# Kernel tuning notes

Hardware: AMD Instinct MI355X
Metric: run time of the kernel (lower is better)

Reference implementation:

```python
import jax, jax.numpy as jnp
import numpy as np

B, E, C, K, H, OUT = 8192, 16, 256, 2, 64, 387

def setup_inputs() -> dict:
    ks = jax.random.split(jax.random.key(0), 6)
    x = jax.random.normal(ks[0], (B, E, C), dtype=jnp.float32)
    adj = jax.random.normal(ks[1], (E, E), dtype=jnp.float32) * (6.0 / (E + E)) ** 0.5  # xavier-ish
    adj_bias = jax.random.normal(ks[2], (1,), dtype=jnp.float32) * 0.1
    cheb_w = jax.random.normal(ks[3], (K * C, H), dtype=jnp.float32) * (6.0 / (K * C + H)) ** 0.5
    brelu_bias = jnp.zeros((1, 1, H), dtype=jnp.float32)
    fc_w = jax.random.normal(ks[4], (OUT, H), dtype=jnp.float32) * (1.0 / H) ** 0.5
    fc_b = jax.random.normal(ks[5], (OUT,), dtype=jnp.float32) * (1.0 / H) ** 0.5
    return {"x": x, "adj": adj, "adj_bias": adj_bias, "cheb_w": cheb_w,
            "brelu_bias": brelu_bias, "fc_w": fc_w, "fc_b": fc_b}

def reference(x, adj, adj_bias, cheb_w, brelu_bias, fc_w, fc_b):
    # adaptive adjacency + biased ReLU (Eq. 4 prelude)
    w = jax.nn.relu(adj + adj_bias)  # (E,E)
    # normalized Laplacian: I - D^{-1/2} W D^{-1/2}
    d_re = 1.0 / jnp.sqrt(jnp.sum(w, axis=1) + 1e-5)  # (E,)
    lap = jnp.eye(E, dtype=x.dtype) - d_re[:, None] * w * d_re[None, :]  # (E,E)
    # Chebyshev polynomial, k=2: T0 = ones, T1 = lap @ x
    t0 = jnp.ones_like(x)                       # (B,E,C)
    t1 = jnp.einsum('ij,bjc->bic', lap, x)      # (B,E,C)
    # torch: stack on dim=1 -> permute(0,2,3,1) -> flatten(2)  == interleave along last axis
    cp = jnp.stack([t0, t1], axis=-1).reshape(B, E, K * C)  # (B,E,K*C)
    h = jnp.einsum('bek,kh->beh', cp, cheb_w)   # (B,E,H)
    # dropout is identity at eval
    h = jax.nn.relu(brelu_bias + h)
    out = jnp.einsum('beh,oh->beo', h, fc_w) + fc_b  # (B,E,OUT)
    return out
```

## Files before the change

kernel.cpp:

```cpp
#include <hip/hip_runtime.h>
#include <stdint.h>


typedef __attribute__((ext_vector_type(4))) float f32x4;
typedef __attribute__((ext_vector_type(8))) short s16x8;
typedef __attribute__((ext_vector_type(4))) short s16x4;

#define WS_CH_B    0
#define WS_LAP_B   256
#define WS_LAPA_B  1280
#define WS_FCB_B   1792
#define WS_W1T2_B  4096
#define WS_FCW2_B  36864

static __device__ __forceinline__ short f2bf(float f) {
    union { float f; uint32_t u; } v; v.f = f;
    uint32_t r = (v.u + 0x7fffu + ((v.u >> 16) & 1u)) >> 16;
    return (short)r;
}

__global__ void prep_kernel(const float* __restrict__ adj,
                            const float* __restrict__ adj_bias,
                            const float* __restrict__ cheb_w,
                            const float* __restrict__ brelu_bias,
                            const float* __restrict__ fc_w,
                            const float* __restrict__ fc_b,
                            char* __restrict__ ws) {
    float* chf  = (float*)(ws + WS_CH_B);
    float* lapf = (float*)(ws + WS_LAP_B);
    short* lapA = (short*)(ws + WS_LAPA_B);
    float* fcbp = (float*)(ws + WS_FCB_B);
    short* w1t2 = (short*)(ws + WS_W1T2_B);
    short* fcw2 = (short*)(ws + WS_FCW2_B);
    int t = threadIdx.x;

    if (blockIdx.x == 0) {
        __shared__ float sw[16][17];
        __shared__ float sdre[16];
        __shared__ float slap[16][16];
        __shared__ float csum[4][64];
        float ab = adj_bias[0];
        {
            int i = t >> 4, j = t & 15;
            sw[i][j] = fmaxf(adj[t] + ab, 0.f);
        }
        {
            int hh = t & 63, part = t >> 6;
            float s = 0.f;
            #pragma unroll 8
            for (int i = 0; i < 64; ++i) s += cheb_w[(2 * (part * 64 + i)) * 64 + hh];
            csum[part][hh] = s;
        }
        __syncthreads();
        if (t < 16) {
            float s = 0.f;
            #pragma unroll
            for (int j = 0; j < 16; ++j) s += sw[t][j];
            sdre[t] = 1.0f / sqrtf(s + 1e-5f);
        }
        __syncthreads();
        {
            int i = t >> 4, j = t & 15;
            float l = (i == j ? 1.f : 0.f) - sdre[i] * sw[i][j] * sdre[j];
            slap[i][j] = l;
            lapf[t] = l;
        }
        __syncthreads();
        if (t < 64) {
            int m = t & 15, qq = t >> 4;
            #pragma unroll
            for (int i = 0; i < 4; ++i)
                lapA[t * 4 + i] = f2bf(slap[m][qq * 4 + i]);
            chf[t] = csum[0][t] + csum[1][t] + csum[2][t] + csum[3][t] + brelu_bias[t];
        }
        for (int o = t; o < 400; o += 256) fcbp[o] = (o < 387) ? fc_b[o] : 0.f;
    }
    int gt = blockIdx.x * blockDim.x + t;
    int nthr = gridDim.x * blockDim.x;
    for (int idx = gt; idx < 32 * 512; idx += nthr) {
        int frag = idx >> 9, r = idx & 511;
        int lane = r >> 3, j = r & 7;
        int kb = frag >> 2, nt = frag & 3;
        int k = kb * 32 + (lane >> 4) * 8 + j;
        int col = nt * 16 + (lane & 15);
        w1t2[idx] = f2bf(cheb_w[(2 * k + 1) * 64 + col]);
    }
    for (int idx = gt; idx < 50 * 512; idx += nthr) {
        int frag = idx >> 9, r = idx & 511;
        int lane = r >> 3, j = r & 7;
        int tt = frag >> 1, f = frag & 1;
        int o = tt * 16 + (lane & 15);
        int k = f * 32 + (lane >> 4) * 8 + j;
        fcw2[idx] = (o < 387) ? f2bf(fc_w[o * 64 + k]) : (short)0;
    }
}

__global__ __launch_bounds__(256) void fused_kernel(
        const float* __restrict__ x,
        const char* __restrict__ ws,
        float* __restrict__ out) {
    const float* chf  = (const float*)(ws + WS_CH_B);
    const short* lapA = (const short*)(ws + WS_LAPA_B);
    const float* fcbp = (const float*)(ws + WS_FCB_B);
    const short* w1t2 = (const short*)(ws + WS_W1T2_B);
    const short* fcw2 = (const short*)(ws + WS_FCW2_B);

    __shared__ __align__(16) short sw1[32 * 512];
    __shared__ __align__(16) short hs[4][16][80];

    const int lane = threadIdx.x & 63;
    const int wave = threadIdx.x >> 6;
    const int n = lane & 15;
    const int q = lane >> 4;
    const long b = (long)blockIdx.x * 4 + wave;

    {
        const s16x8* srcv = (const s16x8*)w1t2;
        s16x8* dstv = (s16x8*)sw1;
        #pragma unroll
        for (int i = 0; i < 8; ++i)
            dstv[i * 256 + threadIdx.x] = srcv[i * 256 + threadIdx.x];
    }

    const float* xrow = x + b * 4096 + n * 256 + q * 8;
    f32x4 xr[16];
    #pragma unroll
    for (int kb = 0; kb < 8; ++kb) {
        xr[2 * kb]     = *(const f32x4*)(xrow + kb * 32);
        xr[2 * kb + 1] = *(const f32x4*)(xrow + kb * 32 + 4);
    }
    s16x8 af[8];
    #pragma unroll
    for (int kb = 0; kb < 8; ++kb) {
        f32x4 xa = xr[2 * kb], xc = xr[2 * kb + 1];
        af[kb][0] = f2bf(xa[0]); af[kb][1] = f2bf(xa[1]);
        af[kb][2] = f2bf(xa[2]); af[kb][3] = f2bf(xa[3]);
        af[kb][4] = f2bf(xc[0]); af[kb][5] = f2bf(xc[1]);
        af[kb][6] = f2bf(xc[2]); af[kb][7] = f2bf(xc[3]);
    }
    __syncthreads();

    const short* w1l = sw1 + lane * 8;
    s16x8 bfr[2][4];
    #pragma unroll
    for (int nt = 0; nt < 4; ++nt)
        bfr[0][nt] = *(const s16x8*)(w1l + nt * 512);
    f32x4 g[4];
    #pragma unroll
    for (int nt = 0; nt < 4; ++nt) g[nt] = (f32x4){0.f, 0.f, 0.f, 0.f};
    #pragma unroll
    for (int kb = 0; kb < 8; ++kb) {
        const int cur = kb & 1;
        if (kb < 7) {
            #pragma unroll
            for (int nt = 0; nt < 4; ++nt)
                bfr[cur ^ 1][nt] = *(const s16x8*)(w1l + ((kb + 1) * 4 + nt) * 512);
        }
        #pragma unroll
        for (int nt = 0; nt < 4; ++nt)
            g[nt] = __builtin_amdgcn_mfma_f32_16x16x32_bf16(af[kb], bfr[cur][nt], g[nt], 0, 0, 0);
    }

    f32x4 h[4];
#if defined(__has_builtin) && __has_builtin(__builtin_amdgcn_mfma_f32_16x16x16bf16_1k)
    {
        s16x4 la = *(const s16x4*)(lapA + lane * 4);
        const f32x4 z4 = (f32x4){0.f, 0.f, 0.f, 0.f};
        #pragma unroll
        for (int nt = 0; nt < 4; ++nt) {
            s16x4 gb;
            gb[0] = f2bf(g[nt][0]); gb[1] = f2bf(g[nt][1]);
            gb[2] = f2bf(g[nt][2]); gb[3] = f2bf(g[nt][3]);
            h[nt] = __builtin_amdgcn_mfma_f32_16x16x16bf16_1k(la, gb, z4, 0, 0, 0);
        }
    }
#else
    {
        __shared__ float gs[4][16][68];
        const float* lapf = (const float*)(ws + WS_LAP_B);
        #pragma unroll
        for (int r = 0; r < 4; ++r) {
            gs[wave][q * 4 + r][0 * 16 + n] = g[0][r];
            gs[wave][q * 4 + r][1 * 16 + n] = g[1][r];
            gs[wave][q * 4 + r][2 * 16 + n] = g[2][r];
            gs[wave][q * 4 + r][3 * 16 + n] = g[3][r];
        }
        __syncthreads();
        #pragma unroll
        for (int nt = 0; nt < 4; ++nt) h[nt] = (f32x4){0.f, 0.f, 0.f, 0.f};
        #pragma unroll
        for (int e = 0; e < 16; ++e) {
            float l0 = lapf[(q * 4 + 0) * 16 + e];
            float l1 = lapf[(q * 4 + 1) * 16 + e];
            float l2 = lapf[(q * 4 + 2) * 16 + e];
            float l3 = lapf[(q * 4 + 3) * 16 + e];
            #pragma unroll
            for (int nt = 0; nt < 4; ++nt) {
                float gv = gs[wave][e][nt * 16 + n];
                h[nt][0] += l0 * gv; h[nt][1] += l1 * gv;
                h[nt][2] += l2 * gv; h[nt][3] += l3 * gv;
            }
        }
    }
#endif

    #pragma unroll
    for (int nt = 0; nt < 4; ++nt) {
        float cv = chf[nt * 16 + n];
        #pragma unroll
        for (int r = 0; r < 4; ++r) {
            float v = fmaxf(h[nt][r] + cv, 0.f);
            hs[wave][q * 4 + r][nt * 16 + n] = f2bf(v);
        }
    }

    const short* fw = fcw2 + lane * 8;
    s16x8 fb[2][2];
    {
        const int tt0 = wave;
        fb[0][0] = *(const s16x8*)(fw + (tt0 * 2 + 0) * 512);
        fb[0][1] = *(const s16x8*)(fw + (tt0 * 2 + 1) * 512);
    }
    asm volatile("s_waitcnt lgkmcnt(0)" ::: "memory");
    __builtin_amdgcn_s_barrier();
    __builtin_amdgcn_sched_barrier(0);

    s16x8 ha[4][2];
    #pragma unroll
    for (int gi = 0; gi < 4; ++gi) {
        ha[gi][0] = *(const s16x8*)(&hs[gi][n][q * 8]);
        ha[gi][1] = *(const s16x8*)(&hs[gi][n][32 + q * 8]);
    }

    const long bbase = (long)blockIdx.x * 4;
    #pragma unroll
    for (int i = 0; i < 7; ++i) {
        const int tt = wave + 4 * i;
        if (tt >= 25) break;
        const int cur = i & 1;
        const int tn = tt + 4;
        if (tn < 25) {
            fb[cur ^ 1][0] = *(const s16x8*)(fw + (tn * 2 + 0) * 512);
            fb[cur ^ 1][1] = *(const s16x8*)(fw + (tn * 2 + 1) * 512);
        }
        const int o = tt * 16 + n;
        const float bias = fcbp[o];
        #pragma unroll
        for (int gi = 0; gi < 4; ++gi) {
            f32x4 acc = (f32x4){bias, bias, bias, bias};
            acc = __builtin_amdgcn_mfma_f32_16x16x32_bf16(ha[gi][0], fb[cur][0], acc, 0, 0, 0);
            acc = __builtin_amdgcn_mfma_f32_16x16x32_bf16(ha[gi][1], fb[cur][1], acc, 0, 0, 0);
            if (o < 387) {
                float* outb = out + ((bbase + gi) * 16 + q * 4) * 387;
                outb[0 * 387 + o] = acc[0];
                outb[1 * 387 + o] = acc[1];
                outb[2 * 387 + o] = acc[2];
                outb[3 * 387 + o] = acc[3];
            }
        }
    }
}

extern "C" void kernel_launch(void* const* d_in, const int* in_sizes, int n_in,
                              void* d_out, int out_size, void* d_ws, size_t ws_size,
                              hipStream_t stream) {
    const float* x          = (const float*)d_in[0];
    const float* adj        = (const float*)d_in[1];
    const float* adj_bias   = (const float*)d_in[2];
    const float* cheb_w     = (const float*)d_in[3];
    const float* brelu_bias = (const float*)d_in[4];
    const float* fc_w       = (const float*)d_in[5];
    const float* fc_b       = (const float*)d_in[6];
    float* outp = (float*)d_out;
    char* ws = (char*)d_ws;

    prep_kernel<<<64, 256, 0, stream>>>(adj, adj_bias, cheb_w, brelu_bias, fc_w, fc_b, ws);
    fused_kernel<<<2048, 256, 0, stream>>>(x, ws, outp);
}
```

Baseline: 343.0 us.

## Process two batch groups per block and prefetch next x tile during compute

Each block now handles two groups of four batch elements instead of one and launches half as many blocks. The shared cheb weight staging, Laplacian fragment, bias and channel constants are loaded once and reused for both groups. The second group's x rows are loaded from global memory while the first group's MFMA work is running. This spreads the per-block setup cost over more work and hides load latency, but it raises register pressure and adds a barrier between the two iterations.

```diff
diff --git a/kernel.cpp b/kernel.cpp
--- a/kernel.cpp
+++ b/kernel.cpp
@@ -112,7 +112,17 @@
     const int wave = threadIdx.x >> 6;
     const int n = lane & 15;
     const int q = lane >> 4;
-    const long b = (long)blockIdx.x * 4 + wave;
+
+    const long grp0 = (long)blockIdx.x * 2;
+    f32x4 xr[16];
+    {
+        const float* xrow = x + (grp0 * 4 + wave) * 4096 + n * 256 + q * 8;
+        #pragma unroll
+        for (int kb = 0; kb < 8; ++kb) {
+            xr[2 * kb]     = *(const f32x4*)(xrow + kb * 32);
+            xr[2 * kb + 1] = *(const f32x4*)(xrow + kb * 32 + 4);
+        }
+    }
 
     {
         const s16x8* srcv = (const s16x8*)w1t2;
@@ -122,142 +132,160 @@
             dstv[i * 256 + threadIdx.x] = srcv[i * 256 + threadIdx.x];
     }
 
-    const float* xrow = x + b * 4096 + n * 256 + q * 8;
-    f32x4 xr[16];
+    const s16x4 la = *(const s16x4*)(lapA + lane * 4);
+    float cv[4];
     #pragma unroll
-    for (int kb = 0; kb < 8; ++kb) {
-        xr[2 * kb]     = *(const f32x4*)(xrow + kb * 32);
-        xr[2 * kb + 1] = *(const f32x4*)(xrow + kb * 32 + 4);
-    }
-    s16x8 af[8];
-    #pragma unroll
-    for (int kb = 0; kb < 8; ++kb) {
-        f32x4 xa = xr[2 * kb], xc = xr[2 * kb + 1];
-        af[kb][0] = f2bf(xa[0]); af[kb][1] = f2bf(xa[1]);
-        af[kb][2] = f2bf(xa[2]); af[kb][3] = f2bf(xa[3]);
-        af[kb][4] = f2bf(xc[0]); af[kb][5] = f2bf(xc[1]);
-        af[kb][6] = f2bf(xc[2]); af[kb][7] = f2bf(xc[3]);
-    }
-    __syncthreads();
-
-    const short* w1l = sw1 + lane * 8;
-    s16x8 bfr[2][4];
-    #pragma unroll
-    for (int nt = 0; nt < 4; ++nt)
-        bfr[0][nt] = *(const s16x8*)(w1l + nt * 512);
-    f32x4 g[4];
-    #pragma unroll
-    for (int nt = 0; nt < 4; ++nt) g[nt] = (f32x4){0.f, 0.f, 0.f, 0.f};
-    #pragma unroll
-    for (int kb = 0; kb < 8; ++kb) {
-        const int cur = kb & 1;
-        if (kb < 7) {
-            #pragma unroll
-            for (int nt = 0; nt < 4; ++nt)
-                bfr[cur ^ 1][nt] = *(const s16x8*)(w1l + ((kb + 1) * 4 + nt) * 512);
-        }
-        #pragma unroll
-        for (int nt = 0; nt < 4; ++nt)
-            g[nt] = __builtin_amdgcn_mfma_f32_16x16x32_bf16(af[kb], bfr[cur][nt], g[nt], 0, 0, 0);
-    }
-
-    f32x4 h[4];
-#if defined(__has_builtin) && __has_builtin(__builtin_amdgcn_mfma_f32_16x16x16bf16_1k)
-    {
-        s16x4 la = *(const s16x4*)(lapA + lane * 4);
-        const f32x4 z4 = (f32x4){0.f, 0.f, 0.f, 0.f};
-        #pragma unroll
-        for (int nt = 0; nt < 4; ++nt) {
-            s16x4 gb;
-            gb[0] = f2bf(g[nt][0]); gb[1] = f2bf(g[nt][1]);
-            gb[2] = f2bf(g[nt][2]); gb[3] = f2bf(g[nt][3]);
-            h[nt] = __builtin_amdgcn_mfma_f32_16x16x16bf16_1k(la, gb, z4, 0, 0, 0);
-        }
-    }
-#else
-    {
-        __shared__ float gs[4][16][68];
-        const float* lapf = (const float*)(ws + WS_LAP_B);
-        #pragma unroll
-        for (int r = 0; r < 4; ++r) {
-            gs[wave][q * 4 + r][0 * 16 + n] = g[0][r];
-            gs[wave][q * 4 + r][1 * 16 + n] = g[1][r];
-            gs[wave][q * 4 + r][2 * 16 + n] = g[2][r];
-            gs[wave][q * 4 + r][3 * 16 + n] = g[3][r];
-        }
-        __syncthreads();
-        #pragma unroll
-        for (int nt = 0; nt < 4; ++nt) h[nt] = (f32x4){0.f, 0.f, 0.f, 0.f};
-        #pragma unroll
-        for (int e = 0; e < 16; ++e) {
-            float l0 = lapf[(q * 4 + 0) * 16 + e];
-            float l1 = lapf[(q * 4 + 1) * 16 + e];
-            float l2 = lapf[(q * 4 + 2) * 16 + e];
-            float l3 = lapf[(q * 4 + 3) * 16 + e];
-            #pragma unroll
-            for (int nt = 0; nt < 4; ++nt) {
-                float gv = gs[wave][e][nt * 16 + n];
-                h[nt][0] += l0 * gv; h[nt][1] += l1 * gv;
-                h[nt][2] += l2 * gv; h[nt][3] += l3 * gv;
-            }
-        }
-    }
-#endif
-
-    #pragma unroll
-    for (int nt = 0; nt < 4; ++nt) {
-        float cv = chf[nt * 16 + n];
-        #pragma unroll
-        for (int r = 0; r < 4; ++r) {
-            float v = fmaxf(h[nt][r] + cv, 0.f);
-            hs[wave][q * 4 + r][nt * 16 + n] = f2bf(v);
-        }
-    }
-
-    const short* fw = fcw2 + lane * 8;
-    s16x8 fb[2][2];
-    {
-        const int tt0 = wave;
-        fb[0][0] = *(const s16x8*)(fw + (tt0 * 2 + 0) * 512);
-        fb[0][1] = *(const s16x8*)(fw + (tt0 * 2 + 1) * 512);
-    }
-    asm volatile("s_waitcnt lgkmcnt(0)" ::: "memory");
-    __builtin_amdgcn_s_barrier();
-    __builtin_amdgcn_sched_barrier(0);
-
-    s16x8 ha[4][2];
-    #pragma unroll
-    for (int gi = 0; gi < 4; ++gi) {
-        ha[gi][0] = *(const s16x8*)(&hs[gi][n][q * 8]);
-        ha[gi][1] = *(const s16x8*)(&hs[gi][n][32 + q * 8]);
-    }
-
-    const long bbase = (long)blockIdx.x * 4;
+    for (int nt = 0; nt < 4; ++nt) cv[nt] = chf[nt * 16 + n];
+    float biasv[7];
     #pragma unroll
     for (int i = 0; i < 7; ++i) {
-        const int tt = wave + 4 * i;
-        if (tt >= 25) break;
-        const int cur = i & 1;
-        const int tn = tt + 4;
-        if (tn < 25) {
-            fb[cur ^ 1][0] = *(const s16x8*)(fw + (tn * 2 + 0) * 512);
-            fb[cur ^ 1][1] = *(const s16x8*)(fw + (tn * 2 + 1) * 512);
-        }
-        const int o = tt * 16 + n;
-        const float bias = fcbp[o];
+        int tt = wave + 4 * i;
+        biasv[i] = (tt < 25) ? fcbp[tt * 16 + n] : 0.f;
+    }
+    const short* w1l = sw1 + lane * 8;
+    const short* fw  = fcw2 + lane * 8;
+
+    #pragma unroll
+    for (int it = 0; it < 2; ++it) {
+        const long b = (grp0 + it) * 4 + wave;
+
+        s16x8 af[8];
+        #pragma unroll
+        for (int kb = 0; kb < 8; ++kb) {
+            f32x4 xa = xr[2 * kb], xc = xr[2 * kb + 1];
+            af[kb][0] = f2bf(xa[0]); af[kb][1] = f2bf(xa[1]);
+            af[kb][2] = f2bf(xa[2]); af[kb][3] = f2bf(xa[3]);
+            af[kb][4] = f2bf(xc[0]); af[kb][5] = f2bf(xc[1]);
+            af[kb][6] = f2bf(xc[2]); af[kb][7] = f2bf(xc[3]);
+        }
+        if (it == 0) __syncthreads();
+
+        s16x8 bfr[2][4];
+        #pragma unroll
+        for (int nt = 0; nt < 4; ++nt)
+            bfr[0][nt] = *(const s16x8*)(w1l + nt * 512);
+        f32x4 g[4];
+        #pragma unroll
+        for (int nt = 0; nt < 4; ++nt) g[nt] = (f32x4){0.f, 0.f, 0.f, 0.f};
+        #pragma unroll
+        for (int kb = 0; kb < 8; ++kb) {
+            const int cur = kb & 1;
+            if (kb < 7) {
+                #pragma unroll
+                for (int nt = 0; nt < 4; ++nt)
+                    bfr[cur ^ 1][nt] = *(const s16x8*)(w1l + ((kb + 1) * 4 + nt) * 512);
+            }
+            #pragma unroll
+            for (int nt = 0; nt < 4; ++nt)
+                g[nt] = __builtin_amdgcn_mfma_f32_16x16x32_bf16(af[kb], bfr[cur][nt], g[nt], 0, 0, 0);
+        }
+
+        if (it == 0) {
+            const float* xrow = x + ((grp0 + 1) * 4 + wave) * 4096 + n * 256 + q * 8;
+            #pragma unroll
+            for (int kb = 0; kb < 8; ++kb) {
+                xr[2 * kb]     = *(const f32x4*)(xrow + kb * 32);
+                xr[2 * kb + 1] = *(const f32x4*)(xrow + kb * 32 + 4);
+            }
+        }
+
+        f32x4 h[4];
+#if defined(__has_builtin) && __has_builtin(__builtin_amdgcn_mfma_f32_16x16x16bf16_1k)
+        {
+            const f32x4 z4 = (f32x4){0.f, 0.f, 0.f, 0.f};
+            #pragma unroll
+            for (int nt = 0; nt < 4; ++nt) {
+                s16x4 gb;
+                gb[0] = f2bf(g[nt][0]); gb[1] = f2bf(g[nt][1]);
+                gb[2] = f2bf(g[nt][2]); gb[3] = f2bf(g[nt][3]);
+                h[nt] = __builtin_amdgcn_mfma_f32_16x16x16bf16_1k(la, gb, z4, 0, 0, 0);
+            }
+        }
+#else
+        {
+            __shared__ float gs[4][16][68];
+            const float* lapf = (const float*)(ws + WS_LAP_B);
+            #pragma unroll
+            for (int r = 0; r < 4; ++r) {
+                gs[wave][q * 4 + r][0 * 16 + n] = g[0][r];
+                gs[wave][q * 4 + r][1 * 16 + n] = g[1][r];
+                gs[wave][q * 4 + r][2 * 16 + n] = g[2][r];
+                gs[wave][q * 4 + r][3 * 16 + n] = g[3][r];
+            }
+            __syncthreads();
+            #pragma unroll
+            for (int nt = 0; nt < 4; ++nt) h[nt] = (f32x4){0.f, 0.f, 0.f, 0.f};
+            #pragma unroll
+            for (int e = 0; e < 16; ++e) {
+                float l0 = lapf[(q * 4 + 0) * 16 + e];
+                float l1 = lapf[(q * 4 + 1) * 16 + e];
+                float l2 = lapf[(q * 4 + 2) * 16 + e];
+                float l3 = lapf[(q * 4 + 3) * 16 + e];
+                #pragma unroll
+                for (int nt = 0; nt < 4; ++nt) {
+                    float gv = gs[wave][e][nt * 16 + n];
+                    h[nt][0] += l0 * gv; h[nt][1] += l1 * gv;
+                    h[nt][2] += l2 * gv; h[nt][3] += l3 * gv;
+                }
+            }
+        }
+#endif
+
+        #pragma unroll
+        for (int nt = 0; nt < 4; ++nt) {
+            #pragma unroll
+            for (int r = 0; r < 4; ++r) {
+                float v = fmaxf(h[nt][r] + cv[nt], 0.f);
+                hs[wave][q * 4 + r][nt * 16 + n] = f2bf(v);
+            }
+        }
+
+        s16x8 fb[2][2];
+        {
+            const int tt0 = wave;
+            fb[0][0] = *(const s16x8*)(fw + (tt0 * 2 + 0) * 512);
+            fb[0][1] = *(const s16x8*)(fw + (tt0 * 2 + 1) * 512);
+        }
+        asm volatile("s_waitcnt lgkmcnt(0)" ::: "memory");
+        __builtin_amdgcn_s_barrier();
+        __builtin_amdgcn_sched_barrier(0);
+
+        s16x8 ha[4][2];
         #pragma unroll
         for (int gi = 0; gi < 4; ++gi) {
-            f32x4 acc = (f32x4){bias, bias, bias, bias};
-            acc = __builtin_amdgcn_mfma_f32_16x16x32_bf16(ha[gi][0], fb[cur][0], acc, 0, 0, 0);
-            acc = __builtin_amdgcn_mfma_f32_16x16x32_bf16(ha[gi][1], fb[cur][1], acc, 0, 0, 0);
-            if (o < 387) {
-                float* outb = out + ((bbase + gi) * 16 + q * 4) * 387;
-                outb[0 * 387 + o] = acc[0];
-                outb[1 * 387 + o] = acc[1];
-                outb[2 * 387 + o] = acc[2];
-                outb[3 * 387 + o] = acc[3];
-            }
-        }
+            ha[gi][0] = *(const s16x8*)(&hs[gi][n][q * 8]);
+            ha[gi][1] = *(const s16x8*)(&hs[gi][n][32 + q * 8]);
+        }
+
+        const long bbase = (grp0 + it) * 4;
+        #pragma unroll
+        for (int i = 0; i < 7; ++i) {
+            const int tt = wave + 4 * i;
+            if (tt >= 25) break;
+            const int cur = i & 1;
+            const int tn = tt + 4;
+            if (tn < 25) {
+                fb[cur ^ 1][0] = *(const s16x8*)(fw + (tn * 2 + 0) * 512);
+                fb[cur ^ 1][1] = *(const s16x8*)(fw + (tn * 2 + 1) * 512);
+            }
+            const int o = tt * 16 + n;
+            const float bias = biasv[i];
+            #pragma unroll
+            for (int gi = 0; gi < 4; ++gi) {
+                f32x4 acc = (f32x4){bias, bias, bias, bias};
+                acc = __builtin_amdgcn_mfma_f32_16x16x32_bf16(ha[gi][0], fb[cur][0], acc, 0, 0, 0);
+                acc = __builtin_amdgcn_mfma_f32_16x16x32_bf16(ha[gi][1], fb[cur][1], acc, 0, 0, 0);
+                if (o < 387) {
+                    float* outb = out + ((bbase + gi) * 16 + q * 4) * 387;
+                    outb[0 * 387 + o] = acc[0];
+                    outb[1 * 387 + o] = acc[1];
+                    outb[2 * 387 + o] = acc[2];
+                    outb[3 * 387 + o] = acc[3];
+                }
+            }
+        }
+
+        if (it == 0) __builtin_amdgcn_s_barrier();
     }
 }
 
@@ -275,5 +303,5 @@
     char* ws = (char*)d_ws;
 
     prep_kernel<<<64, 256, 0, stream>>>(adj, adj_bias, cheb_w, brelu_bias, fc_w, fc_b, ws);
-    fused_kernel<<<2048, 256, 0, stream>>>(x, ws, outp);
+    fused_kernel<<<1024, 256, 0, stream>>>(x, ws, outp);
 }
```

Measured after the change: 343.5 us. About the same (+0.1%).
